# Performance work log

Measured on AMD Instinct MI355X. Metric: run time of the kernel, lower is better.

The kernel has to match this reference:

```python
import jax, jax.numpy as jnp
import numpy as np

N_NODES = 50000
N_EDGES = 800000
IN_C, HID_C, OUT_C = 128, 128, 64


def setup_inputs() -> dict:
    key = jax.random.key(0)
    ks = jax.random.split(key, 8)
    x = jax.random.normal(ks[0], (N_NODES, IN_C), dtype=jnp.float32)
    edge_index = jax.random.randint(ks[1], (2, N_EDGES), 0, N_NODES, dtype=jnp.int64)
    s = 1.0 / np.sqrt(IN_C)
    W1_l = jax.random.uniform(ks[2], (HID_C, IN_C), jnp.float32, -s, s)
    W1_r = jax.random.uniform(ks[3], (HID_C, IN_C), jnp.float32, -s, s)
    b1 = jnp.zeros((HID_C,), jnp.float32)
    s2 = 1.0 / np.sqrt(HID_C)
    W2_l = jax.random.uniform(ks[4], (OUT_C, HID_C), jnp.float32, -s2, s2)
    W2_r = jax.random.uniform(ks[5], (OUT_C, HID_C), jnp.float32, -s2, s2)
    b2 = jnp.zeros((OUT_C,), jnp.float32)
    return {"x": x, "edge_index": edge_index, "W1_l": W1_l, "W1_r": W1_r,
            "b1": b1, "W2_l": W2_l, "W2_r": W2_r, "b2": b2}


def _sage_conv(x, src, dst, W_l, W_r, b, n_nodes):
    # mean aggregation of source-node features onto target nodes
    agg = jax.ops.segment_sum(x[src], dst, num_segments=n_nodes)  # [N, d]
    deg = jax.ops.segment_sum(jnp.ones((src.shape[0],), x.dtype), dst,
                              num_segments=n_nodes)               # [N]
    agg = agg / jnp.maximum(deg, 1.0)[:, None]
    # out = lin_l(agg) + lin_r(x) + bias (PyG SAGEConv, root_weight=True)
    return agg @ W_l.T + x @ W_r.T + b


def reference(x, edge_index, W1_l, W1_r, b1, W2_l, W2_r, b2):
    src, dst = edge_index[0], edge_index[1]
    n = x.shape[0]
    h = _sage_conv(x, src, dst, W1_l, W1_r, b1, n)
    h = jax.nn.relu(h)
    # dropout is identity in eval mode (training=False)
    out = _sage_conv(h, src, dst, W2_l, W2_r, b2, n)
    return jax.nn.log_softmax(out, axis=1)
```

## Files before the change

### kernel.cpp

```cpp
#include <hip/hip_runtime.h>
#include <hip/hip_bf16.h>

#define IN_C  128
#define HID_C 128
#define OUT_C 64
#define PAD   48
#define BPAD  2560
#define EPB   4096
#define MAX_NBUCK 512

typedef __attribute__((ext_vector_type(8))) short short8;
typedef __attribute__((ext_vector_type(4))) float f32x4;

__device__ __forceinline__ unsigned short f2bf(float f) {
  unsigned int u = __float_as_uint(f);
  unsigned int r = (u + 0x7fffu + ((u >> 16) & 1u)) >> 16;
  return (unsigned short)r;
}
__device__ __forceinline__ float bflo(unsigned int v) { return __uint_as_float(v << 16); }
__device__ __forceinline__ float bfhi(unsigned int v) { return __uint_as_float(v & 0xffff0000u); }
__device__ __forceinline__ float bf2f(unsigned short u) { return __uint_as_float((unsigned int)u << 16); }

__global__ __launch_bounds__(256) void k_prep(const float* __restrict__ X,
                                              const float* __restrict__ W1l,
                                              const float* __restrict__ W1r,
                                              const float* __restrict__ W2l,
                                              const float* __restrict__ W2r,
                                              unsigned short* __restrict__ Xb,
                                              unsigned short* __restrict__ Wb1,
                                              unsigned short* __restrict__ Wb2,
                                              int* __restrict__ gcur,
                                              int n4, int nb) {
  int i = blockIdx.x * 256 + threadIdx.x;
  if (i < n4) {
    float4 v = ((const float4*)X)[i];
    uint2 o;
    o.x = (unsigned int)f2bf(v.x) | ((unsigned int)f2bf(v.y) << 16);
    o.y = (unsigned int)f2bf(v.z) | ((unsigned int)f2bf(v.w) << 16);
    ((uint2*)Xb)[i] = o;
    return;
  }
  int j = i - n4;
  if (j < 128 * 256) {
    int o = j >> 8, k = j & 255;
    float v = (k < 128) ? W1l[o * 128 + k] : W1r[o * 128 + (k - 128)];
    Wb1[j] = f2bf(v);
    return;
  }
  int k2 = j - 128 * 256;
  if (k2 < 128 * 128) {
    int o = k2 >> 7, k = k2 & 127;
    float v = (o < 64) ? W2l[o * 128 + k] : W2r[(o - 64) * 128 + k];
    Wb2[k2] = f2bf(v);
    return;
  }
  int l = k2 - 128 * 128;
  if (l < nb) gcur[l] = 0;
}

__global__ __launch_bounds__(256) void k_bucket2(const int* __restrict__ src,
                                                 const int* __restrict__ dst,
                                                 int* __restrict__ gcur,
                                                 unsigned int* __restrict__ buckets,
                                                 int nE, int nb) {
  __shared__ int hist[MAX_NBUCK];
  __shared__ int base[MAX_NBUCK];
  const int e0 = blockIdx.x * EPB;
  const int e1 = min(e0 + EPB, nE);
  for (int i = threadIdx.x; i < nb; i += 256) hist[i] = 0;
  __syncthreads();
  for (int e = e0 + threadIdx.x; e < e1; e += 256)
    atomicAdd(&hist[dst[e] >> 7], 1);
  __syncthreads();
  for (int i = threadIdx.x; i < nb; i += 256) {
    int c = hist[i];
    base[i] = (c > 0) ? atomicAdd(&gcur[i], c) : 0;
    hist[i] = 0;
  }
  __syncthreads();
  for (int e = e0 + threadIdx.x; e < e1; e += 256) {
    int d = dst[e];
    int b = d >> 7;
    int pos = base[b] + atomicAdd(&hist[b], 1);
    if (pos < BPAD)
      buckets[(size_t)b * BPAD + pos] = ((unsigned int)(d & 127) << 16) | (unsigned int)src[e];
  }
}

__global__ __launch_bounds__(256) void k_csr(const unsigned int* __restrict__ buckets,
                                             const int* __restrict__ bcnt,
                                             int* __restrict__ cnt,
                                             unsigned short* __restrict__ csr, int n) {
  __shared__ int lc[128];
  __shared__ unsigned short lcsr[128 * PAD];
  const int b = blockIdx.x;
  const int base = b << 7;
  const int lim = min(128, n - base);
  const int m = min(bcnt[b], BPAD);
  for (int i = threadIdx.x; i < 128; i += 256) lc[i] = 0;
  __syncthreads();
  const unsigned int* bk = buckets + (size_t)b * BPAD;
  for (int i = threadIdx.x; i < m; i += 256) {
    unsigned int p = bk[i];
    int d = p >> 16;
    int pos = atomicAdd(&lc[d], 1);
    if (pos < PAD) lcsr[d * PAD + pos] = (unsigned short)(p & 0xffffu);
  }
  __syncthreads();
  for (int i = threadIdx.x; i < lim; i += 256) cnt[base + i] = min(lc[i], PAD) | (lc[i] << 8);
  unsigned int* co = (unsigned int*)(csr + (size_t)base * PAD);
  const unsigned int* ci = (const unsigned int*)lcsr;
  const int nu = lim * PAD / 2;
  for (int i = threadIdx.x; i < nu; i += 256) co[i] = ci[i];
}

__global__ __launch_bounds__(256) void k_gather(const unsigned short* __restrict__ Xb,
                                                const int* __restrict__ cnt,
                                                const unsigned short* __restrict__ csr,
                                                unsigned short* __restrict__ aggb, int n) {
  const int lane = threadIdx.x & 63;
  const int node = blockIdx.x * 4 + __builtin_amdgcn_readfirstlane(threadIdx.x >> 6);
  if (node >= n) return;
  const int c = cnt[node];
  const int deg = c >> 8;
  const int m = c & 255;
  const unsigned short* rw = csr + (size_t)node * PAD;
  const unsigned int* Xp = (const unsigned int*)Xb;
  float ax = 0.0f, ay = 0.0f;
  int e = 0;
  for (; e + 4 <= m; e += 4) {
    int s0 = rw[e + 0], s1 = rw[e + 1], s2 = rw[e + 2], s3 = rw[e + 3];
    unsigned int a = Xp[(size_t)s0 * 64 + lane];
    unsigned int b = Xp[(size_t)s1 * 64 + lane];
    unsigned int c2 = Xp[(size_t)s2 * 64 + lane];
    unsigned int d = Xp[(size_t)s3 * 64 + lane];
    ax += (bflo(a) + bflo(b)) + (bflo(c2) + bflo(d));
    ay += (bfhi(a) + bfhi(b)) + (bfhi(c2) + bfhi(d));
  }
  for (; e < m; ++e) {
    unsigned int a = Xp[(size_t)rw[e] * 64 + lane];
    ax += bflo(a);
    ay += bfhi(a);
  }
  const float invd = 1.0f / fmaxf((float)deg, 1.0f);
  unsigned int o = (unsigned int)f2bf(ax * invd) | ((unsigned int)f2bf(ay * invd) << 16);
  ((unsigned int*)aggb)[(size_t)node * 64 + lane] = o;
}

__global__ __launch_bounds__(512) void k_gemm1(
    const unsigned short* __restrict__ aggb, const unsigned short* __restrict__ xb,
    const unsigned short* __restrict__ Wb,
    const float* __restrict__ bias,
    unsigned short* __restrict__ hb, int nRows)
{
  __shared__ unsigned short wlds[128 * 256];

  const int lane = threadIdx.x & 63;
  const int w = threadIdx.x >> 6;
  const int lr = lane & 15;
  const int kg = lane >> 4;
  const int sw = lr & 7;
  const int r0 = blockIdx.x * 128 + w * 16;
  int arow = r0 + lr;
  if (arow >= nRows) arow = nRows - 1;

  short8 aA[4], aX[4];
#pragma unroll
  for (int kc = 0; kc < 4; ++kc) {
    aA[kc] = *(const short8*)(aggb + (size_t)arow * 128 + kc * 32 + kg * 8);
    aX[kc] = *(const short8*)(xb   + (size_t)arow * 128 + kc * 32 + kg * 8);
  }

  {
    const uint4* gw = (const uint4*)Wb;
    uint4* lw = (uint4*)wlds;
#pragma unroll
    for (int t = 0; t < 8; ++t) {
      int i = threadIdx.x + t * 512;
      int row = i >> 5, c = i & 31;
      lw[(row << 5) | (c ^ (row & 7))] = gw[i];
    }
  }
  __syncthreads();

  f32x4 acc[8];
#pragma unroll
  for (int ct = 0; ct < 8; ++ct) acc[ct] = (f32x4)(0.0f);

#pragma unroll
  for (int ct = 0; ct < 8; ++ct) {
    const unsigned short* wrowp = wlds + ((ct * 16 + lr) << 8);
#pragma unroll
    for (int kc = 0; kc < 4; ++kc) {
      short8 b0 = *(const short8*)(wrowp + ((((kc * 4 + kg) ^ sw)) << 3));
      acc[ct] = __builtin_amdgcn_mfma_f32_16x16x32_bf16(aA[kc], b0, acc[ct], 0, 0, 0);
    }
#pragma unroll
    for (int kc = 0; kc < 4; ++kc) {
      short8 b1 = *(const short8*)(wrowp + (((16 + ((kc * 4 + kg) ^ sw))) << 3));
      acc[ct] = __builtin_amdgcn_mfma_f32_16x16x32_bf16(aX[kc], b1, acc[ct], 0, 0, 0);
    }
  }

#pragma unroll
  for (int ct = 0; ct < 8; ++ct) {
    const int col = ct * 16 + lr;
    const float b = bias[col];
#pragma unroll
    for (int v = 0; v < 4; ++v) {
      int row = r0 + kg * 4 + v;
      if (row < nRows) {
        float o = fmaxf(acc[ct][v] + b, 0.0f);
        hb[(size_t)row * 128 + col] = f2bf(o);
      }
    }
  }
}

__global__ __launch_bounds__(512) void k_gemm2t(
    const unsigned short* __restrict__ hb,
    const unsigned short* __restrict__ Wb,
    unsigned short* __restrict__ pq, int nRows)
{
  __shared__ unsigned short wlds[128 * 128];

  const int lane = threadIdx.x & 63;
  const int w = threadIdx.x >> 6;
  const int lr = lane & 15;
  const int kg = lane >> 4;
  const int sw = lr & 7;
  const int r0 = blockIdx.x * 128 + w * 16;
  int arow = r0 + lr;
  if (arow >= nRows) arow = nRows - 1;

  short8 aH[4];
#pragma unroll
  for (int kc = 0; kc < 4; ++kc)
    aH[kc] = *(const short8*)(hb + (size_t)arow * 128 + kc * 32 + kg * 8);

  {
    const uint4* gw = (const uint4*)Wb;
    uint4* lw = (uint4*)wlds;
#pragma unroll
    for (int t = 0; t < 4; ++t) {
      int i = threadIdx.x + t * 512;
      int row = i >> 4, c = i & 15;
      lw[(row << 4) | (c ^ (row & 7))] = gw[i];
    }
  }
  __syncthreads();

  f32x4 acc[8];
#pragma unroll
  for (int ct = 0; ct < 8; ++ct) acc[ct] = (f32x4)(0.0f);

#pragma unroll
  for (int ct = 0; ct < 8; ++ct) {
    const unsigned short* wrowp = wlds + ((ct * 16 + lr) << 7);
#pragma unroll
    for (int kc = 0; kc < 4; ++kc) {
      short8 b0 = *(const short8*)(wrowp + ((((kc * 4 + kg) ^ sw)) << 3));
      acc[ct] = __builtin_amdgcn_mfma_f32_16x16x32_bf16(aH[kc], b0, acc[ct], 0, 0, 0);
    }
  }

#pragma unroll
  for (int ct = 0; ct < 8; ++ct) {
    const int col = ct * 16 + lr;
#pragma unroll
    for (int v = 0; v < 4; ++v) {
      int row = r0 + kg * 4 + v;
      if (row < nRows)
        pq[(size_t)row * 128 + col] = f2bf(acc[ct][v]);
    }
  }
}

__global__ __launch_bounds__(256) void k_gather2sm(const unsigned short* __restrict__ pq,
                                                   const int* __restrict__ cnt,
                                                   const unsigned short* __restrict__ csr,
                                                   const float* __restrict__ bias,
                                                   float* __restrict__ OUT, int n) {
  const int lane = threadIdx.x & 63;
  const int node = blockIdx.x * 4 + __builtin_amdgcn_readfirstlane(threadIdx.x >> 6);
  if (node >= n) return;
  const int c = cnt[node];
  const int deg = c >> 8;
  const int m = c & 255;
  const unsigned short* rw = csr + (size_t)node * PAD;

  float a = 0.0f;
  int e = 0;
  for (; e + 4 <= m; e += 4) {
    int s0 = rw[e + 0], s1 = rw[e + 1], s2 = rw[e + 2], s3 = rw[e + 3];
    float v0 = bf2f(pq[(size_t)s0 * 128 + lane]);
    float v1 = bf2f(pq[(size_t)s1 * 128 + lane]);
    float v2 = bf2f(pq[(size_t)s2 * 128 + lane]);
    float v3 = bf2f(pq[(size_t)s3 * 128 + lane]);
    a += (v0 + v1) + (v2 + v3);
  }
  for (; e < m; ++e)
    a += bf2f(pq[(size_t)rw[e] * 128 + lane]);

  a *= 1.0f / fmaxf((float)deg, 1.0f);
  float v = a + bf2f(pq[(size_t)node * 128 + 64 + lane]) + bias[lane];

  float mx = v;
#pragma unroll
  for (int mask = 1; mask < 64; mask <<= 1) mx = fmaxf(mx, __shfl_xor(mx, mask));
  float s = __expf(v - mx);
#pragma unroll
  for (int mask = 1; mask < 64; mask <<= 1) s += __shfl_xor(s, mask);
  OUT[(size_t)node * 64 + lane] = v - mx - __logf(s);
}

extern "C" void kernel_launch(void* const* d_in, const int* in_sizes, int n_in,
                              void* d_out, int out_size, void* d_ws, size_t ws_size,
                              hipStream_t stream) {
  const float* x   = (const float*)d_in[0];
  const int*   ei  = (const int*)d_in[1];
  const float* W1l = (const float*)d_in[2];
  const float* W1r = (const float*)d_in[3];
  const float* b1  = (const float*)d_in[4];
  const float* W2l = (const float*)d_in[5];
  const float* W2r = (const float*)d_in[6];
  const float* b2  = (const float*)d_in[7];
  float* out = (float*)d_out;

  const int N  = in_sizes[0] / IN_C;
  const int nE = in_sizes[1] / 2;
  const int* src = ei;
  const int* dst = ei + nE;

  const int nb = (N + 127) >> 7;
  const int nPad = nb << 7;

  char* w = (char*)d_ws;
  size_t off = 0;
  int* cnt             = (int*)(w + off); off += ((size_t)nPad * 4 + 255) & ~255ull;
  int* gcur            = (int*)(w + off); off += ((size_t)nb * 4 + 255) & ~255ull;
  unsigned int* bkts   = (unsigned int*)(w + off); off += (size_t)nb * BPAD * 4;
  unsigned short* csr  = (unsigned short*)(w + off); off += ((size_t)nPad * PAD * 2 + 255) & ~255ull;
  unsigned short* xb   = (unsigned short*)(w + off); off += (size_t)N * 128 * 2;
  unsigned short* hb   = (unsigned short*)(w + off); off += (size_t)N * 128 * 2;
  unsigned short* aggb = (unsigned short*)(w + off); off += (size_t)N * 128 * 2;
  unsigned short* Wb1  = (unsigned short*)(w + off); off += 128 * 256 * 2;
  unsigned short* Wb2  = (unsigned short*)(w + off); off += 128 * 128 * 2;
  unsigned short* pq   = aggb;

  const int n4 = N * 128 / 4;
  const int prep_items = n4 + 128 * 256 + 128 * 128 + nb;

  k_prep<<<(prep_items + 255) / 256, 256, 0, stream>>>(x, W1l, W1r, W2l, W2r,
                                                       xb, Wb1, Wb2, gcur, n4, nb);

  k_bucket2<<<(nE + EPB - 1) / EPB, 256, 0, stream>>>(src, dst, gcur, bkts, nE, nb);
  k_csr<<<nb, 256, 0, stream>>>(bkts, gcur, cnt, csr, N);

  k_gather<<<(N + 3) / 4, 256, 0, stream>>>(xb, cnt, csr, aggb, N);
  k_gemm1<<<(N + 127) / 128, 512, 0, stream>>>(aggb, xb, Wb1, b1, hb, N);

  k_gemm2t<<<(N + 127) / 128, 512, 0, stream>>>(hb, Wb2, pq, N);
  k_gather2sm<<<(N + 3) / 4, 256, 0, stream>>>(pq, cnt, csr, b2, out, N);
}
```

Baseline: 130.3 us.

## Fuse edge bucketing into prep kernel with per-block bucket cells and vectorized gathers

```diff
diff --git a/kernel.cpp b/kernel.cpp
--- a/kernel.cpp
+++ b/kernel.cpp
@@ -5,8 +5,8 @@
 #define HID_C 128
 #define OUT_C 64
 #define PAD   48
-#define BPAD  2560
 #define EPB   4096
+#define CAP   40
 #define MAX_NBUCK 512
 
 typedef __attribute__((ext_vector_type(8))) short short8;
@@ -21,17 +21,38 @@
 __device__ __forceinline__ float bfhi(unsigned int v) { return __uint_as_float(v & 0xffff0000u); }
 __device__ __forceinline__ float bf2f(unsigned short u) { return __uint_as_float((unsigned int)u << 16); }
 
-__global__ __launch_bounds__(256) void k_prep(const float* __restrict__ X,
-                                              const float* __restrict__ W1l,
-                                              const float* __restrict__ W1r,
-                                              const float* __restrict__ W2l,
-                                              const float* __restrict__ W2r,
-                                              unsigned short* __restrict__ Xb,
-                                              unsigned short* __restrict__ Wb1,
-                                              unsigned short* __restrict__ Wb2,
-                                              int* __restrict__ gcur,
-                                              int n4, int nb) {
-  int i = blockIdx.x * 256 + threadIdx.x;
+__global__ __launch_bounds__(256) void k_bucket3(
+    const int* __restrict__ src, const int* __restrict__ dst,
+    const float* __restrict__ X,
+    const float* __restrict__ W1l, const float* __restrict__ W1r,
+    const float* __restrict__ W2l, const float* __restrict__ W2r,
+    unsigned short* __restrict__ ccnt,
+    unsigned int* __restrict__ bkts,
+    unsigned short* __restrict__ Xb,
+    unsigned short* __restrict__ Wb1, unsigned short* __restrict__ Wb2,
+    int nE, int nb, int n4, int nbk)
+{
+  __shared__ int cur[MAX_NBUCK];
+  const int blk = blockIdx.x;
+  if (blk < nbk) {
+    for (int i = threadIdx.x; i < nb; i += 256) cur[i] = 0;
+    __syncthreads();
+    const int e0 = blk * EPB;
+    const int e1 = min(e0 + EPB, nE);
+    for (int e = e0 + threadIdx.x; e < e1; e += 256) {
+      int d = dst[e];
+      int b = d >> 7;
+      int p = atomicAdd(&cur[b], 1);
+      if (p < CAP)
+        bkts[((size_t)blk * nb + b) * CAP + p] =
+            ((unsigned int)(d & 127) << 16) | (unsigned int)src[e];
+    }
+    __syncthreads();
+    for (int i = threadIdx.x; i < nb; i += 256)
+      ccnt[(size_t)blk * nb + i] = (unsigned short)cur[i];
+    return;
+  }
+  int i = (blk - nbk) * 256 + threadIdx.x;
   if (i < n4) {
     float4 v = ((const float4*)X)[i];
     uint2 o;
@@ -52,65 +73,36 @@
     int o = k2 >> 7, k = k2 & 127;
     float v = (o < 64) ? W2l[o * 128 + k] : W2r[(o - 64) * 128 + k];
     Wb2[k2] = f2bf(v);
-    return;
-  }
-  int l = k2 - 128 * 128;
-  if (l < nb) gcur[l] = 0;
-}
-
-__global__ __launch_bounds__(256) void k_bucket2(const int* __restrict__ src,
-                                                 const int* __restrict__ dst,
-                                                 int* __restrict__ gcur,
-                                                 unsigned int* __restrict__ buckets,
-                                                 int nE, int nb) {
-  __shared__ int hist[MAX_NBUCK];
-  __shared__ int base[MAX_NBUCK];
-  const int e0 = blockIdx.x * EPB;
-  const int e1 = min(e0 + EPB, nE);
-  for (int i = threadIdx.x; i < nb; i += 256) hist[i] = 0;
-  __syncthreads();
-  for (int e = e0 + threadIdx.x; e < e1; e += 256)
-    atomicAdd(&hist[dst[e] >> 7], 1);
-  __syncthreads();
-  for (int i = threadIdx.x; i < nb; i += 256) {
-    int c = hist[i];
-    base[i] = (c > 0) ? atomicAdd(&gcur[i], c) : 0;
-    hist[i] = 0;
-  }
-  __syncthreads();
-  for (int e = e0 + threadIdx.x; e < e1; e += 256) {
-    int d = dst[e];
-    int b = d >> 7;
-    int pos = base[b] + atomicAdd(&hist[b], 1);
-    if (pos < BPAD)
-      buckets[(size_t)b * BPAD + pos] = ((unsigned int)(d & 127) << 16) | (unsigned int)src[e];
-  }
-}
-
-__global__ __launch_bounds__(256) void k_csr(const unsigned int* __restrict__ buckets,
-                                             const int* __restrict__ bcnt,
-                                             int* __restrict__ cnt,
-                                             unsigned short* __restrict__ csr, int n) {
+  }
+}
+
+__global__ __launch_bounds__(256) void k_csr2(const unsigned int* __restrict__ bkts,
+                                              const unsigned short* __restrict__ ccnt,
+                                              int* __restrict__ cnt,
+                                              unsigned short* __restrict__ csr,
+                                              int n, int nbk, int nb) {
   __shared__ int lc[128];
   __shared__ unsigned short lcsr[128 * PAD];
   const int b = blockIdx.x;
   const int base = b << 7;
   const int lim = min(128, n - base);
-  const int m = min(bcnt[b], BPAD);
   for (int i = threadIdx.x; i < 128; i += 256) lc[i] = 0;
   __syncthreads();
-  const unsigned int* bk = buckets + (size_t)b * BPAD;
-  for (int i = threadIdx.x; i < m; i += 256) {
-    unsigned int p = bk[i];
-    int d = p >> 16;
-    int pos = atomicAdd(&lc[d], 1);
-    if (pos < PAD) lcsr[d * PAD + pos] = (unsigned short)(p & 0xffffu);
+  for (int j = threadIdx.x; j < nbk; j += 256) {
+    int mj = min((int)ccnt[(size_t)j * nb + b], CAP);
+    const unsigned int* cell = bkts + ((size_t)j * nb + b) * CAP;
+    for (int i = 0; i < mj; ++i) {
+      unsigned int p = cell[i];
+      int d = p >> 16;
+      int pos = atomicAdd(&lc[d], 1);
+      if (pos < PAD) lcsr[d * PAD + pos] = (unsigned short)(p & 0xffffu);
+    }
   }
   __syncthreads();
   for (int i = threadIdx.x; i < lim; i += 256) cnt[base + i] = min(lc[i], PAD) | (lc[i] << 8);
-  unsigned int* co = (unsigned int*)(csr + (size_t)base * PAD);
-  const unsigned int* ci = (const unsigned int*)lcsr;
-  const int nu = lim * PAD / 2;
+  uint4* co = (uint4*)(csr + (size_t)base * PAD);
+  const uint4* ci = (const uint4*)lcsr;
+  const int nu = lim * 6;
   for (int i = threadIdx.x; i < nu; i += 256) co[i] = ci[i];
 }
 
@@ -124,24 +116,24 @@
   const int c = cnt[node];
   const int deg = c >> 8;
   const int m = c & 255;
-  const unsigned short* rw = csr + (size_t)node * PAD;
+  const short8* rwv = (const short8*)(csr + (size_t)node * PAD);
   const unsigned int* Xp = (const unsigned int*)Xb;
   float ax = 0.0f, ay = 0.0f;
-  int e = 0;
-  for (; e + 4 <= m; e += 4) {
-    int s0 = rw[e + 0], s1 = rw[e + 1], s2 = rw[e + 2], s3 = rw[e + 3];
-    unsigned int a = Xp[(size_t)s0 * 64 + lane];
-    unsigned int b = Xp[(size_t)s1 * 64 + lane];
-    unsigned int c2 = Xp[(size_t)s2 * 64 + lane];
-    unsigned int d = Xp[(size_t)s3 * 64 + lane];
-    ax += (bflo(a) + bflo(b)) + (bflo(c2) + bflo(d));
-    ay += (bfhi(a) + bfhi(b)) + (bfhi(c2) + bfhi(d));
-  }
-  for (; e < m; ++e) {
-    unsigned int a = Xp[(size_t)rw[e] * 64 + lane];
-    ax += bflo(a);
-    ay += bfhi(a);
-  }
+
+#define G1_GROUP(g)                                                          \
+  if ((g) * 8 < m) {                                                         \
+    short8 I = rwv[g];                                                       \
+    unsigned int v[8];                                                       \
+    _Pragma("unroll") for (int t = 0; t < 8; ++t) {                          \
+      int s = ((g) * 8 + t < m) ? (int)(unsigned short)I[t] : 0;             \
+      v[t] = Xp[(size_t)s * 64 + lane];                                      \
+    }                                                                        \
+    _Pragma("unroll") for (int t = 0; t < 8; ++t)                            \
+      if ((g) * 8 + t < m) { ax += bflo(v[t]); ay += bfhi(v[t]); }           \
+  }
+  G1_GROUP(0) G1_GROUP(1) G1_GROUP(2) G1_GROUP(3) G1_GROUP(4) G1_GROUP(5)
+#undef G1_GROUP
+
   const float invd = 1.0f / fmaxf((float)deg, 1.0f);
   unsigned int o = (unsigned int)f2bf(ax * invd) | ((unsigned int)f2bf(ay * invd) << 16);
   ((unsigned int*)aggb)[(size_t)node * 64 + lane] = o;
@@ -287,20 +279,22 @@
   const int c = cnt[node];
   const int deg = c >> 8;
   const int m = c & 255;
-  const unsigned short* rw = csr + (size_t)node * PAD;
+  const short8* rwv = (const short8*)(csr + (size_t)node * PAD);
 
   float a = 0.0f;
-  int e = 0;
-  for (; e + 4 <= m; e += 4) {
-    int s0 = rw[e + 0], s1 = rw[e + 1], s2 = rw[e + 2], s3 = rw[e + 3];
-    float v0 = bf2f(pq[(size_t)s0 * 128 + lane]);
-    float v1 = bf2f(pq[(size_t)s1 * 128 + lane]);
-    float v2 = bf2f(pq[(size_t)s2 * 128 + lane]);
-    float v3 = bf2f(pq[(size_t)s3 * 128 + lane]);
-    a += (v0 + v1) + (v2 + v3);
-  }
-  for (; e < m; ++e)
-    a += bf2f(pq[(size_t)rw[e] * 128 + lane]);
+#define G2_GROUP(g)                                                          \
+  if ((g) * 8 < m) {                                                         \
+    short8 I = rwv[g];                                                       \
+    float v[8];                                                              \
+    _Pragma("unroll") for (int t = 0; t < 8; ++t) {                          \
+      int s = ((g) * 8 + t < m) ? (int)(unsigned short)I[t] : 0;             \
+      v[t] = bf2f(pq[(size_t)s * 128 + lane]);                               \
+    }                                                                        \
+    _Pragma("unroll") for (int t = 0; t < 8; ++t)                            \
+      if ((g) * 8 + t < m) a += v[t];                                        \
+  }
+  G2_GROUP(0) G2_GROUP(1) G2_GROUP(2) G2_GROUP(3) G2_GROUP(4) G2_GROUP(5)
+#undef G2_GROUP
 
   a *= 1.0f / fmaxf((float)deg, 1.0f);
   float v = a + bf2f(pq[(size_t)node * 128 + 64 + lane]) + bias[lane];
@@ -332,14 +326,15 @@
   const int* src = ei;
   const int* dst = ei + nE;
 
-  const int nb = (N + 127) >> 7;
+  const int nb  = (N + 127) >> 7;
   const int nPad = nb << 7;
+  const int nbk = (nE + EPB - 1) / EPB;
 
   char* w = (char*)d_ws;
   size_t off = 0;
   int* cnt             = (int*)(w + off); off += ((size_t)nPad * 4 + 255) & ~255ull;
-  int* gcur            = (int*)(w + off); off += ((size_t)nb * 4 + 255) & ~255ull;
-  unsigned int* bkts   = (unsigned int*)(w + off); off += (size_t)nb * BPAD * 4;
+  unsigned short* ccnt = (unsigned short*)(w + off); off += ((size_t)nbk * nb * 2 + 255) & ~255ull;
+  unsigned int* bkts   = (unsigned int*)(w + off); off += (size_t)nbk * nb * CAP * 4;
   unsigned short* csr  = (unsigned short*)(w + off); off += ((size_t)nPad * PAD * 2 + 255) & ~255ull;
   unsigned short* xb   = (unsigned short*)(w + off); off += (size_t)N * 128 * 2;
   unsigned short* hb   = (unsigned short*)(w + off); off += (size_t)N * 128 * 2;
@@ -349,13 +344,13 @@
   unsigned short* pq   = aggb;
 
   const int n4 = N * 128 / 4;
-  const int prep_items = n4 + 128 * 256 + 128 * 128 + nb;
-
-  k_prep<<<(prep_items + 255) / 256, 256, 0, stream>>>(x, W1l, W1r, W2l, W2r,
-                                                       xb, Wb1, Wb2, gcur, n4, nb);
-
-  k_bucket2<<<(nE + EPB - 1) / EPB, 256, 0, stream>>>(src, dst, gcur, bkts, nE, nb);
-  k_csr<<<nb, 256, 0, stream>>>(bkts, gcur, cnt, csr, N);
+  const int prep_items = n4 + 128 * 256 + 128 * 128;
+  const int grid_b3 = nbk + (prep_items + 255) / 256;
+
+  k_bucket3<<<grid_b3, 256, 0, stream>>>(src, dst, x, W1l, W1r, W2l, W2r,
+                                         ccnt, bkts, xb, Wb1, Wb2, nE, nb, n4, nbk);
+
+  k_csr2<<<nb, 256, 0, stream>>>(bkts, ccnt, cnt, csr, N, nbk, nb);
 
   k_gather<<<(N + 3) / 4, 256, 0, stream>>>(xb, cnt, csr, aggb, N);
   k_gemm1<<<(N + 127) / 128, 512, 0, stream>>>(aggb, xb, Wb1, b1, hb, N);
```

Measured after the change: 110.3 us. 1.18x faster.
